# Kernel tuning notes

Measured on AMD Instinct MI355X. Metric: run time of the kernel, lower is better.

## Reference

```python
import jax, jax.numpy as jnp
import numpy as np

K = 2          # kernel_size
NQ = 4         # n_qubits = K*K
NL = 2         # n_layers


def setup_inputs() -> dict:
    key = jax.random.key(0)
    ks = jax.random.split(key, 6)
    x = jax.random.uniform(ks[0], (64, 1, 128, 128), jnp.float32, 0.0, np.pi)
    conv_w = jax.random.normal(ks[1], (1, 1, K, K), jnp.float32) * 0.5
    conv_b = jax.random.normal(ks[2], (1,), jnp.float32) * 0.1
    ry_angles = jax.random.normal(ks[3], (NL, NQ), jnp.float32)  # fixed RY params
    head_w = jax.random.normal(ks[4], (1, 2), jnp.float32) * 0.5
    head_b = jax.random.normal(ks[5], (1,), jnp.float32) * 0.1
    return {"x": x, "conv_w": conv_w, "conv_b": conv_b,
            "ry_angles": ry_angles, "head_w": head_w, "head_b": head_b}


def _rx(state, theta, wire):
    # state: (N, 2,2,2,2) complex; theta: (N,) batched angle
    ax = wire + 1
    st = jnp.moveaxis(state, ax, 1)
    s0, s1 = st[:, 0], st[:, 1]                      # (N, 2,2,2)
    c = jnp.cos(theta * 0.5).reshape((-1, 1, 1, 1))
    s = jnp.sin(theta * 0.5).reshape((-1, 1, 1, 1))
    n0 = c * s0 - 1j * s * s1
    n1 = -1j * s * s0 + c * s1
    return jnp.moveaxis(jnp.stack([n0, n1], axis=1), 1, ax)


def _ry(state, phi, wire):
    # phi: scalar shared angle
    ax = wire + 1
    st = jnp.moveaxis(state, ax, 1)
    s0, s1 = st[:, 0], st[:, 1]
    c = jnp.cos(phi * 0.5)
    s = jnp.sin(phi * 0.5)
    n0 = c * s0 - s * s1
    n1 = s * s0 + c * s1
    return jnp.moveaxis(jnp.stack([n0, n1], axis=1), 1, ax)


def _cnot(state, ctrl, tgt):
    ca, ta = ctrl + 1, tgt + 1
    st = jnp.moveaxis(state, (ca, ta), (1, 2))       # (N, 2, 2, rest)
    new = jnp.stack([st[:, 0], st[:, 1, ::-1]], axis=1)  # flip target where ctrl=1
    return jnp.moveaxis(new, (1, 2), (ca, ta))


def _quantum_expval_z0(patch_flat, ry_angles):
    # patch_flat: (N, 4) -> expval PauliZ(wire 0), shape (N,)
    N = patch_flat.shape[0]
    state = jnp.zeros((N, 2, 2, 2, 2), jnp.complex64).at[:, 0, 0, 0, 0].set(1.0)
    for w in range(NQ):
        state = _rx(state, patch_flat[:, w], w)
    for l in range(NL):
        for w in range(NQ):
            state = _ry(state, ry_angles[l, w], w)
        for w in range(0, NQ - 1, 2):
            state = _cnot(state, w, w + 1)
    p = jnp.real(state) ** 2 + jnp.imag(state) ** 2   # (N,2,2,2,2)
    return p[:, 0].sum(axis=(1, 2, 3)) - p[:, 1].sum(axis=(1, 2, 3))


def reference(x, conv_w, conv_b, ry_angles, head_w, head_b):
    B, _, H, W = x.shape
    # all KxK sliding patches, feature order (c, kh, kw) row-major == patch.view(-1)
    patches = jax.lax.conv_general_dilated_patches(x, (K, K), (1, 1), 'VALID')  # (B,4,Ph,Pw)
    Ph, Pw = patches.shape[2], patches.shape[3]
    pf = patches.transpose(0, 2, 3, 1).reshape(-1, K * K)   # (N, 4)
    conv_out = pf @ conv_w.reshape(K * K) + conv_b[0]       # (N,)
    q_out = _quantum_expval_z0(pf, ry_angles)               # (N,)
    per_patch = head_w[0, 0] * conv_out + head_w[0, 1] * q_out + head_b[0]
    out = per_patch.reshape(B, Ph * Pw).mean(axis=1)        # mean over windows
    return out[:, None]
```

## Files before the change

kernel.cpp:

```cpp
#include <hip/hip_runtime.h>
#include <math.h>


#define XH 128
#define XW 128
#define PW 127
#define NP (127 * 127)
#define NB 64
#define SLICES 32
#define PPB ((NP + SLICES - 1) / SLICES)
#define BLK1 256

__device__ __forceinline__ void circuit_coeffs(const float* __restrict__ ry,
                                               float k[5]) {
    float U[4][4] = {{1,0,0,0},{0,1,0,0},{0,0,1,0},{0,0,0,1}};
    for (int l = 0; l < 2; ++l) {
        float c0 = cosf(0.5f * ry[l*4+0]), s0 = sinf(0.5f * ry[l*4+0]);
        float c1 = cosf(0.5f * ry[l*4+1]), s1 = sinf(0.5f * ry[l*4+1]);
        for (int q1 = 0; q1 < 2; ++q1)
            for (int c = 0; c < 4; ++c) {
                float a = U[q1][c], d = U[2+q1][c];
                U[q1][c]   = c0*a - s0*d;
                U[2+q1][c] = s0*a + c0*d;
            }
        for (int m = 0; m < 2; ++m)
            for (int c = 0; c < 4; ++c) {
                float a = U[2*m][c], d = U[2*m+1][c];
                U[2*m][c]   = c1*a - s1*d;
                U[2*m+1][c] = s1*a + c1*d;
            }
        for (int c = 0; c < 4; ++c) { float t = U[2][c]; U[2][c] = U[3][c]; U[3][c] = t; }
    }
    float pA=0, pB=0, pC=0, pD=0, pAD=0, pBC=0;
    for (int r = 0; r < 4; ++r) {
        float g = (r < 2) ? 1.f : -1.f;
        pA  += g * U[r][0] * U[r][0];
        pB  += g * U[r][1] * U[r][1];
        pC  += g * U[r][2] * U[r][2];
        pD  += g * U[r][3] * U[r][3];
        pAD += g * U[r][0] * U[r][3];
        pBC += g * U[r][1] * U[r][2];
    }
    k[0] = 0.25f * (pA + pB + pC + pD);
    k[1] = 0.25f * (pA + pB - pC - pD);
    k[2] = 0.25f * (pA - pB + pC - pD);
    k[3] = 0.25f * (pA - pB - pC + pD);
    k[4] = 0.50f * (pBC - pAD);
}

__global__ __launch_bounds__(BLK1) void partial_kernel(
    const float* __restrict__ x,
    const float* __restrict__ conv_w,
    const float* __restrict__ head_w,
    const float* __restrict__ ry,
    float* __restrict__ ws)
{
    __shared__ float sk[5];
    __shared__ float red[BLK1 / 64];
    const int tid   = threadIdx.x;
    const int slice = blockIdx.x;
    const int img   = blockIdx.y;

    if (tid == 0) {
        float k[5];
        circuit_coeffs(ry, k);
        for (int i = 0; i < 5; ++i) sk[i] = k[i];
    }
    __syncthreads();

    const float w0 = conv_w[0], w1 = conv_w[1], w2 = conv_w[2], w3 = conv_w[3];
    const float hw0 = head_w[0], hw1 = head_w[1];
    const float k1 = sk[1], k2 = sk[2], k3 = sk[3], k4 = sk[4];

    const float* __restrict__ xb = x + (size_t)img * XH * XW;
    const int p0 = slice * PPB;
    const int p1 = (p0 + PPB < NP) ? p0 + PPB : NP;

    float acc = 0.f;
    for (int p = p0 + tid; p < p1; p += BLK1) {
        int i = p / PW;
        int j = p - i * PW;
        float x00 = xb[i * XW + j];
        float x01 = xb[i * XW + j + 1];
        float x10 = xb[(i + 1) * XW + j];
        float x11 = xb[(i + 1) * XW + j + 1];
        float conv = w0 * x00 + w1 * x01 + w2 * x10 + w3 * x11;
        float s0, c0, s1, c1;
        __sincosf(x00, &s0, &c0);
        __sincosf(x01, &s1, &c1);
        acc += hw0 * conv + hw1 * (k1 * c0 + k2 * c1 + k3 * c0 * c1 + k4 * s0 * s1);
    }

    for (int off = 32; off > 0; off >>= 1)
        acc += __shfl_down(acc, off, 64);
    if ((tid & 63) == 0) red[tid >> 6] = acc;
    __syncthreads();
    if (tid == 0) {
        float t = 0.f;
        for (int w = 0; w < BLK1 / 64; ++w) t += red[w];
        ws[img * SLICES + slice] = t;
    }
}

__global__ __launch_bounds__(64) void final_kernel(
    const float* __restrict__ ws,
    const float* __restrict__ conv_b,
    const float* __restrict__ ry,
    const float* __restrict__ head_w,
    const float* __restrict__ head_b,
    float* __restrict__ out)
{
    const int b = threadIdx.x;
    float k[5];
    circuit_coeffs(ry, k);
    float sum = 0.f;
    for (int s = 0; s < SLICES; ++s) sum += ws[b * SLICES + s];
    const float cconst = head_w[0] * conv_b[0] + head_w[1] * k[0] + head_b[0];
    out[b] = sum * (1.0f / NP) + cconst;
}

extern "C" void kernel_launch(void* const* d_in, const int* in_sizes, int n_in,
                              void* d_out, int out_size, void* d_ws, size_t ws_size,
                              hipStream_t stream) {
    const float* x      = (const float*)d_in[0];
    const float* conv_w = (const float*)d_in[1];
    const float* conv_b = (const float*)d_in[2];
    const float* ry     = (const float*)d_in[3];
    const float* head_w = (const float*)d_in[4];
    const float* head_b = (const float*)d_in[5];
    float* out = (float*)d_out;
    float* ws  = (float*)d_ws;

    dim3 grid1(SLICES, NB);
    partial_kernel<<<grid1, BLK1, 0, stream>>>(x, conv_w, head_w, ry, ws);
    final_kernel<<<1, 64, 0, stream>>>(ws, conv_b, ry, head_w, head_b, out);
}
```

Before: 69.79 us.

## Process one image row per wavefront, load each pixel once, fold conv sum

Restructures the partial kernel so that each wavefront handles one 128-pixel input row, with each lane reading one float2. Because the conv term is linear, it is rewritten as per-pixel weights that depend on the row and column boundaries, so every pixel is read once instead of four times. The sincos of the neighbouring pixel comes from a shuffle rather than being recomputed. Every thread now computes the circuit coefficients itself, which removes the shared-memory broadcast and one barrier, and head weights are folded into the constants.

```diff
diff --git a/kernel.cpp b/kernel.cpp
--- a/kernel.cpp
+++ b/kernel.cpp
@@ -2,21 +2,20 @@
 #include <math.h>
 
 
-#define XH 128
 #define XW 128
-#define PW 127
 #define NP (127 * 127)
 #define NB 64
-#define SLICES 32
-#define PPB ((NP + SLICES - 1) / SLICES)
-#define BLK1 256
+#define RPB 4
+#define NBLK 32
+#define BLK 256
 
 __device__ __forceinline__ void circuit_coeffs(const float* __restrict__ ry,
                                                float k[5]) {
     float U[4][4] = {{1,0,0,0},{0,1,0,0},{0,0,1,0},{0,0,0,1}};
     for (int l = 0; l < 2; ++l) {
-        float c0 = cosf(0.5f * ry[l*4+0]), s0 = sinf(0.5f * ry[l*4+0]);
-        float c1 = cosf(0.5f * ry[l*4+1]), s1 = sinf(0.5f * ry[l*4+1]);
+        float s0, c0, s1, c1;
+        __sincosf(0.5f * ry[l*4+0], &s0, &c0);
+        __sincosf(0.5f * ry[l*4+1], &s1, &c1);
         for (int q1 = 0; q1 < 2; ++q1)
             for (int c = 0; c < 4; ++c) {
                 float a = U[q1][c], d = U[2+q1][c];
@@ -48,62 +47,62 @@
     k[4] = 0.50f * (pBC - pAD);
 }
 
-__global__ __launch_bounds__(BLK1) void partial_kernel(
+__global__ __launch_bounds__(BLK) void row_kernel(
     const float* __restrict__ x,
     const float* __restrict__ conv_w,
     const float* __restrict__ head_w,
     const float* __restrict__ ry,
-    float* __restrict__ ws)
+    float* __restrict__ part)
 {
-    __shared__ float sk[5];
-    __shared__ float red[BLK1 / 64];
-    const int tid   = threadIdx.x;
-    const int slice = blockIdx.x;
-    const int img   = blockIdx.y;
+    __shared__ float red[BLK / 64];
 
-    if (tid == 0) {
-        float k[5];
-        circuit_coeffs(ry, k);
-        for (int i = 0; i < 5; ++i) sk[i] = k[i];
-    }
-    __syncthreads();
+    const int tid  = threadIdx.x;
+    const int lane = tid & 63;
+    const int wave = tid >> 6;
+    const int img  = blockIdx.y;
+    const int row  = blockIdx.x * RPB + wave;
 
-    const float w0 = conv_w[0], w1 = conv_w[1], w2 = conv_w[2], w3 = conv_w[3];
+    float k[5];
+    circuit_coeffs(ry, k);
     const float hw0 = head_w[0], hw1 = head_w[1];
-    const float k1 = sk[1], k2 = sk[2], k3 = sk[3], k4 = sk[4];
+    const float k1 = hw1 * k[1], k2 = hw1 * k[2];
+    const float k3 = hw1 * k[3], k4 = hw1 * k[4];
+    const float w0 = hw0 * conv_w[0], w1 = hw0 * conv_w[1];
+    const float w2 = hw0 * conv_w[2], w3 = hw0 * conv_w[3];
 
-    const float* __restrict__ xb = x + (size_t)img * XH * XW;
-    const int p0 = slice * PPB;
-    const int p1 = (p0 + PPB < NP) ? p0 + PPB : NP;
+    const float P = (row < 127 ? w0 : 0.f) + (row > 0 ? w2 : 0.f);
+    const float Q = (row < 127 ? w1 : 0.f) + (row > 0 ? w3 : 0.f);
 
-    float acc = 0.f;
-    for (int p = p0 + tid; p < p1; p += BLK1) {
-        int i = p / PW;
-        int j = p - i * PW;
-        float x00 = xb[i * XW + j];
-        float x01 = xb[i * XW + j + 1];
-        float x10 = xb[(i + 1) * XW + j];
-        float x11 = xb[(i + 1) * XW + j + 1];
-        float conv = w0 * x00 + w1 * x01 + w2 * x10 + w3 * x11;
+    const float2* __restrict__ xr =
+        (const float2*)(x + ((size_t)img * 128 + row) * XW);
+    const float2 e = xr[lane];
+
+    float acc = e.x * (P + (lane > 0 ? Q : 0.f))
+              + e.y * (Q + (lane < 63 ? P : 0.f));
+
+    if (row < 127) {
         float s0, c0, s1, c1;
-        __sincosf(x00, &s0, &c0);
-        __sincosf(x01, &s1, &c1);
-        acc += hw0 * conv + hw1 * (k1 * c0 + k2 * c1 + k3 * c0 * c1 + k4 * s0 * s1);
+        __sincosf(e.x, &s0, &c0);
+        __sincosf(e.y, &s1, &c1);
+        float cn = __shfl_down(c0, 1, 64);
+        float sn = __shfl_down(s0, 1, 64);
+        acc += k1 * c0 + k2 * c1 + k3 * c0 * c1 + k4 * s0 * s1;
+        if (lane < 63)
+            acc += k1 * c1 + k2 * cn + k3 * c1 * cn + k4 * s1 * sn;
     }
 
     for (int off = 32; off > 0; off >>= 1)
         acc += __shfl_down(acc, off, 64);
-    if ((tid & 63) == 0) red[tid >> 6] = acc;
+    if (lane == 0) red[wave] = acc;
     __syncthreads();
     if (tid == 0) {
-        float t = 0.f;
-        for (int w = 0; w < BLK1 / 64; ++w) t += red[w];
-        ws[img * SLICES + slice] = t;
+        float t = red[0] + red[1] + red[2] + red[3];
+        part[img * NBLK + blockIdx.x] = t;
     }
 }
 
 __global__ __launch_bounds__(64) void final_kernel(
-    const float* __restrict__ ws,
+    const float* __restrict__ part,
     const float* __restrict__ conv_b,
     const float* __restrict__ ry,
     const float* __restrict__ head_w,
@@ -114,7 +113,7 @@
     float k[5];
     circuit_coeffs(ry, k);
     float sum = 0.f;
-    for (int s = 0; s < SLICES; ++s) sum += ws[b * SLICES + s];
+    for (int s = 0; s < NBLK; ++s) sum += part[b * NBLK + s];
     const float cconst = head_w[0] * conv_b[0] + head_w[1] * k[0] + head_b[0];
     out[b] = sum * (1.0f / NP) + cconst;
 }
@@ -128,10 +127,10 @@
     const float* ry     = (const float*)d_in[3];
     const float* head_w = (const float*)d_in[4];
     const float* head_b = (const float*)d_in[5];
-    float* out = (float*)d_out;
-    float* ws  = (float*)d_ws;
+    float* out  = (float*)d_out;
+    float* part = (float*)d_ws;
 
-    dim3 grid1(SLICES, NB);
-    partial_kernel<<<grid1, BLK1, 0, stream>>>(x, conv_w, head_w, ry, ws);
-    final_kernel<<<1, 64, 0, stream>>>(ws, conv_b, ry, head_w, head_b, out);
+    dim3 grid(NBLK, NB);
+    row_kernel<<<grid, BLK, 0, stream>>>(x, conv_w, head_w, ry, part);
+    final_kernel<<<1, 64, 0, stream>>>(part, conv_b, ry, head_w, head_b, out);
 }
```

Result: no change. 68.74 us (-1.5%).
